# Kernel optimization log

Measured on AMD Instinct MI355X. Metric: run time of the kernel, lower is better.

Reference implementation:

```python
import jax, jax.numpy as jnp
import numpy as np

TOKEN_SELF_ATTN_VALUE = -50000.0
EPS_NORM = 1e-12
EPS_SCATTER = 1e-5
COMMITMENT = 1e-4


def _l2norm(x):
    return x / jnp.maximum(jnp.linalg.norm(x, axis=-1, keepdims=True), EPS_NORM)


def _shift(x):
    # relative-position shift, faithful to the torch `shift` helper
    # x: [..., i, j] -> [..., i, j]
    *pre, i, j = x.shape
    x = jnp.concatenate([x, jnp.zeros((*pre, i, i), x.dtype)], axis=-1)  # [..., i, i+j]
    l = i + j - 1
    x = x.reshape(*pre, i * (i + j))
    pad = (-x.shape[-1]) % l
    x = jnp.concatenate([x, jnp.zeros((*pre, pad), x.dtype)], axis=-1)
    x = x.reshape(*pre, -1, l)
    return x[..., :i, i - 1:]


def setup_inputs() -> dict:
    key = jax.random.key(0)
    k1, k2, k3, k4 = jax.random.split(key, 4)
    b, h, t, d = 4, 8, 8192, 64
    c, wsz = 64, 128
    qk = jax.random.normal(k1, (b, h, t, d), jnp.float32)
    v = jax.random.normal(k2, (b, h, t, d), jnp.float32)
    means = jax.random.normal(k3, (h, c, d), jnp.float32)
    means = _l2norm(means)  # trained kmeans means are unit-normalized
    rel_w = jax.random.normal(k4, (wsz, h, d), jnp.float32) * 0.02
    return {"qk": qk, "v": v, "means": means, "rel_w": rel_w}


def reference(qk, v, means, rel_w):
    b, h, t, d = qk.shape
    c = means.shape[1]
    wsz = min(rel_w.shape[0], t)

    # ---- kmeans routing (eval path: no iterations, fixed means) ----
    k_routing = _l2norm(qk)                                   # [b,h,t,d]
    dists = jnp.einsum('bhld,hcd->bhlc', k_routing, means)    # cosine sims
    buckets = jnp.argmax(dists, axis=-1)                      # [b,h,t]
    # top-wsz tokens per cluster, sorted ascending (matches topk -> sort -> transpose)
    _, idx = jax.lax.top_k(jnp.swapaxes(dists, -1, -2), wsz)  # [b,h,c,wsz]
    indices = jnp.sort(idx, axis=-1).reshape(b, h, c * wsz)   # [b,h,c*wsz]

    # commitment loss against routed means (means is a non-trainable buffer)
    routed_means = means[jnp.arange(h)[None, :, None], buckets]  # [b,h,t,d]
    loss = jnp.mean((k_routing - routed_means) ** 2) * COMMITMENT

    # ---- gather routed windows ----
    qk_g = jnp.take_along_axis(qk, indices[..., None], axis=2).reshape(b, h, c, wsz, d)
    v_g = jnp.take_along_axis(v, indices[..., None], axis=2).reshape(b, h, c, wsz, d)
    q = qk_g
    k = _l2norm(qk_g)

    scale = d ** -0.5
    dots = jnp.einsum('bhnid,bhnjd->bhnij', q, k) * scale     # [b,h,c,wsz,wsz]
    rel = jnp.einsum('bhnid,jhd->bhnij', q, rel_w) * scale
    dots = dots + _shift(rel)

    # token cannot attend to itself within its window
    eye = jnp.eye(wsz, dtype=bool)
    dots = jnp.where(eye, TOKEN_SELF_ATTN_VALUE, dots)

    attn = jax.nn.softmax(dots, axis=-1)
    bo = jnp.einsum('bhnij,bhnjd->bhnid', attn, v_g).reshape(b, h, c * wsz, d)

    # ---- scatter-mean back to original token positions ----
    def scat(idx1, src1):  # idx1: [N], src1: [N,d]
        num = jnp.zeros((t, d), src1.dtype).at[idx1].add(src1)
        den = jnp.zeros((t, d), src1.dtype).at[idx1].add(jnp.ones_like(src1))
        return num / (den + EPS_SCATTER)

    out = jax.vmap(jax.vmap(scat))(indices, bo)               # [b,h,t,d]
    return out, loss
```

## Files before the change

kernel.cpp:

```cpp
#include <hip/hip_runtime.h>
#include <hip/hip_bf16.h>
#include <math.h>

#define NB 4
#define NH 8
#define TT 8192
#define DD 64
#define NC 64
#define WW 128
#define BHN 32
#define SCALE 0.125f
#define INVCAP 24
#define DTPB 64

typedef __bf16  bf16x8 __attribute__((ext_vector_type(8)));
typedef __bf16  bf16x4 __attribute__((ext_vector_type(4)));
typedef float   f32x4  __attribute__((ext_vector_type(4)));
typedef unsigned long long u64;
typedef unsigned int u32;

#define MFMA(a, b, c) __builtin_amdgcn_mfma_f32_16x16x32_bf16((a), (b), (c), 0, 0, 0)

__device__ __forceinline__ u32 monokey(float f) {
    const u32 u = __float_as_uint(f);
    return u ^ (((u32)((int)u >> 31)) | 0x80000000u);
}

#define QD_ADDR(row, gi) (((row) << 6) + ((((gi) ^ ((row) & 7))) << 3))

__global__ __launch_bounds__(256) void k_dists(
    const float* __restrict__ qk, const float* __restrict__ means,
    const float* __restrict__ rel_w, __bf16* __restrict__ relb,
    u32* __restrict__ keys, double* __restrict__ lossa)
{
    __shared__ __attribute__((aligned(16))) __bf16 qh[64 * 64], qm[64 * 64], ql[64 * 64];
    __shared__ __attribute__((aligned(16))) __bf16 ah[64 * 64], am[64 * 64], al[64 * 64];
    __shared__ float invS[DTPB], s2S[DTPB], mn2S[NC];
    __shared__ double red[4];

    const int bh = blockIdx.x, h = bh & 7, tid = threadIdx.x;
    const int t0 = blockIdx.y * DTPB;

    if (blockIdx.y == 0) {
        const float4* rw = (const float4*)rel_w;
#pragma unroll
        for (int k = 0; k < 2; k++) {
            const int i = bh * 512 + k * 256 + tid;
            const float4 v = rw[i];
            bf16x4 o;
            o[0] = (__bf16)v.x; o[1] = (__bf16)v.y; o[2] = (__bf16)v.z; o[3] = (__bf16)v.w;
            *(bf16x4*)(relb + i * 4) = o;
        }
    }

    {
        const int r = tid >> 2, qt = tid & 3;
        const float4* src = (const float4*)(means + (size_t)(h * NC + r) * DD + qt * 16);
        float4 f[4];
        f[0] = src[0]; f[1] = src[1]; f[2] = src[2]; f[3] = src[3];
        bf16x8 vh[2], vm[2], vl[2];
        float ssq = 0.f;
#pragma unroll
        for (int j = 0; j < 16; j++) {
            const float xx = ((const float*)f)[j];
            ssq = fmaf(xx, xx, ssq);
            const __bf16 hh_ = (__bf16)xx;
            const float r1 = xx - (float)hh_;
            const __bf16 mm_ = (__bf16)r1;
            const float r2 = r1 - (float)mm_;
            vh[j >> 3][j & 7] = hh_; vm[j >> 3][j & 7] = mm_; vl[j >> 3][j & 7] = (__bf16)r2;
        }
#pragma unroll
        for (int gg = 0; gg < 2; gg++) {
            const int dst = QD_ADDR(r, qt * 2 + gg);
            *(bf16x8*)(ah + dst) = vh[gg];
            *(bf16x8*)(am + dst) = vm[gg];
            *(bf16x8*)(al + dst) = vl[gg];
        }
        ssq += __shfl_xor(ssq, 1);
        ssq += __shfl_xor(ssq, 2);
        if (qt == 0) mn2S[r] = ssq;
    }
    {
        const int r = tid >> 2, qt = tid & 3;
        const float4* src = (const float4*)(qk + ((size_t)bh * TT + t0 + r) * DD + qt * 16);
        float4 f[4];
        f[0] = src[0]; f[1] = src[1]; f[2] = src[2]; f[3] = src[3];
        bf16x8 vh[2], vm[2], vl[2];
        float ssq = 0.f;
#pragma unroll
        for (int j = 0; j < 16; j++) {
            const float xx = ((const float*)f)[j];
            ssq = fmaf(xx, xx, ssq);
            const __bf16 hh_ = (__bf16)xx;
            const float r1 = xx - (float)hh_;
            const __bf16 mm_ = (__bf16)r1;
            const float r2 = r1 - (float)mm_;
            vh[j >> 3][j & 7] = hh_; vm[j >> 3][j & 7] = mm_; vl[j >> 3][j & 7] = (__bf16)r2;
        }
#pragma unroll
        for (int gg = 0; gg < 2; gg++) {
            const int dst = QD_ADDR(r, qt * 2 + gg);
            *(bf16x8*)(qh + dst) = vh[gg];
            *(bf16x8*)(qm + dst) = vm[gg];
            *(bf16x8*)(ql + dst) = vl[gg];
        }
        ssq += __shfl_xor(ssq, 1);
        ssq += __shfl_xor(ssq, 2);
        if (qt == 0) {
            const float inv = 1.0f / fmaxf(sqrtf(ssq), 1e-12f);
            invS[r] = inv;
            s2S[r] = ssq * inv * inv;
        }
    }
    __syncthreads();

    const int lane = tid & 63, wv = tid >> 6;
    const int lo = lane & 15, quad = lane >> 4;

    bf16x8 Bh[2], Bm[2], Bl[2];
    {
        const int row = wv * 16 + lo;
#pragma unroll
        for (int kh = 0; kh < 2; kh++) {
            const int src = QD_ADDR(row, kh * 4 + quad);
            Bh[kh] = *(const bf16x8*)(qh + src);
            Bm[kh] = *(const bf16x8*)(qm + src);
            Bl[kh] = *(const bf16x8*)(ql + src);
        }
    }

    f32x4 acc[4];
#pragma unroll
    for (int ct = 0; ct < 4; ct++) {
        bf16x8 Ah[2], Am[2], Al[2];
#pragma unroll
        for (int kh = 0; kh < 2; kh++) {
            const int src = QD_ADDR(ct * 16 + lo, kh * 4 + quad);
            Ah[kh] = *(const bf16x8*)(ah + src);
            Am[kh] = *(const bf16x8*)(am + src);
            Al[kh] = *(const bf16x8*)(al + src);
        }
        f32x4 a = (f32x4){0.f, 0.f, 0.f, 0.f};
        a = MFMA(Al[0], Bm[0], a); a = MFMA(Al[1], Bm[1], a);
        a = MFMA(Am[0], Bl[0], a); a = MFMA(Am[1], Bl[1], a);
        a = MFMA(Am[0], Bm[0], a); a = MFMA(Am[1], Bm[1], a);
        a = MFMA(Ah[0], Bl[0], a); a = MFMA(Ah[1], Bl[1], a);
        a = MFMA(Al[0], Bh[0], a); a = MFMA(Al[1], Bh[1], a);
        a = MFMA(Am[0], Bh[0], a); a = MFMA(Am[1], Bh[1], a);
        a = MFMA(Ah[0], Bm[0], a); a = MFMA(Ah[1], Bm[1], a);
        a = MFMA(Ah[0], Bh[0], a); a = MFMA(Ah[1], Bh[1], a);
        acc[ct] = a;
    }

    const int tok = wv * 16 + lo;
    const float inv = invS[tok];
    float rawmax = -3.0e38f; int cbest = 0;
    u32* kout = keys + (size_t)bh * NC * TT + (size_t)(t0 + tok);
#pragma unroll
    for (int ct = 0; ct < 4; ct++)
#pragma unroll
        for (int r = 0; r < 4; r++) {
            const float raw = acc[ct][r];
            const int c = ct * 16 + quad * 4 + r;
            if (raw > rawmax) { rawmax = raw; cbest = c; }
            kout[(size_t)c * TT] = monokey(raw * inv);
        }

#pragma unroll
    for (int off = 16; off < 64; off <<= 1) {
        const float ov = __shfl_xor(rawmax, off);
        const int   oc = __shfl_xor(cbest, off);
        if (ov > rawmax || (ov == rawmax && oc < cbest)) { rawmax = ov; cbest = oc; }
    }
    double lt_lane = 0.0;
    if (quad == 0)
        lt_lane = (double)(s2S[tok] + mn2S[cbest] - 2.0f * rawmax * inv);

#pragma unroll
    for (int o = 32; o; o >>= 1) lt_lane += __shfl_xor(lt_lane, o);
    if (lane == 0) red[wv] = lt_lane;
    __syncthreads();
    if (tid == 0) atomicAdd(lossa, red[0] + red[1] + red[2] + red[3]);
}

__global__ __launch_bounds__(256) void k_topk(
    const u32* __restrict__ keys, int* __restrict__ indices,
    unsigned int* __restrict__ cnt, unsigned short* __restrict__ inv)
{
    __shared__ unsigned int hist[4][256];
    __shared__ int wsum[8];
    __shared__ int bc_bin, bc_rank, bc_cnt;

    const int bhc = blockIdx.x, tid = threadIdx.x;
    const int wv = tid >> 6, lane = tid & 63;
    const int bh = bhc >> 6;

    u32 key[32];
    {
        const uint4* p = (const uint4*)(keys + (size_t)bhc * TT + tid * 32);
#pragma unroll
        for (int i = 0; i < 8; i++) {
            uint4 u = p[i];
            key[4*i] = u.x; key[4*i+1] = u.y; key[4*i+2] = u.z; key[4*i+3] = u.w;
        }
    }

    u32 thr = 0;
    int need = 128, gshift = 24, prevShift = 0;
    unsigned int* hb = &hist[0][0];

    for (int level = 0; level < 4; level++) {
        const int shift = 24 - 8 * level;
        hb[tid] = 0; hb[tid + 256] = 0; hb[tid + 512] = 0; hb[tid + 768] = 0;
        __syncthreads();
        unsigned int* hw = hist[wv];
        if (level == 0) {
#pragma unroll
            for (int i = 0; i < 32; i++)
                atomicAdd(&hw[key[i] >> 24], 1u);
        } else {
            const u32 pv = thr >> prevShift;
#pragma unroll
            for (int i = 0; i < 32; i++)
                if ((key[i] >> prevShift) == pv)
                    atomicAdd(&hw[(key[i] >> shift) & 255u], 1u);
        }
        __syncthreads();

        const int b = 255 - tid;
        const int c = hist[0][b] + hist[1][b] + hist[2][b] + hist[3][b];
        int incl = c;
#pragma unroll
        for (int o = 1; o < 64; o <<= 1) {
            const int v = __shfl_up(incl, o);
            if (lane >= o) incl += v;
        }
        if (lane == 63) wsum[wv] = incl;
        __syncthreads();
        int above = incl - c;
        for (int wj = 0; wj < wv; wj++) above += wsum[wj];
        if (above < need && above + c >= need) {
            bc_bin = b; bc_rank = above; bc_cnt = c;
        }
        __syncthreads();
        thr |= ((u32)bc_bin) << shift;
        need -= bc_rank;
        gshift = shift;
        prevShift = shift;
        if (bc_cnt == need || shift == 0) break;
    }

    const u32 tg = thr >> gshift;
    int cgt = 0, ceq = 0;
#pragma unroll
    for (int i = 0; i < 32; i++) {
        const u32 kg = key[i] >> gshift;
        cgt += (kg > tg) ? 1 : 0;
        ceq += (kg == tg) ? 1 : 0;
    }
    int ig = cgt, ie = ceq;
#pragma unroll
    for (int o = 1; o < 64; o <<= 1) {
        const int vg = __shfl_up(ig, o);
        const int ve = __shfl_up(ie, o);
        if (lane >= o) { ig += vg; ie += ve; }
    }
    if (lane == 63) { wsum[wv] = ig; wsum[4 + wv] = ie; }
    __syncthreads();
    int pgt = ig - cgt, peq = ie - ceq;
    for (int wj = 0; wj < wv; wj++) { pgt += wsum[wj]; peq += wsum[4 + wj]; }

    const int rneed = need;
    int* outp = indices + bhc * WW;
    unsigned int* cntb = cnt + (bh << 13);
    unsigned short* invb = inv + (((size_t)bh << 13) * INVCAP);
    const int cbase = (bhc & 63) * WW;
    int g = 0, e = 0;
#pragma unroll
    for (int i = 0; i < 32; i++) {
        const int tok = tid * 32 + i;
        const u32 kg = key[i] >> gshift;
        if (kg > tg) {
            const int tb = (peq + e < rneed) ? (peq + e) : rneed;
            const int wpos = pgt + g + tb;
            outp[wpos] = tok;
            const unsigned int pos = atomicAdd(&cntb[tok], 1u);
            if (pos < INVCAP) invb[(size_t)tok * INVCAP + pos] = (unsigned short)(cbase + wpos);
            g++;
        } else if (kg == tg) {
            if (peq + e < rneed) {
                const int wpos = pgt + g + peq + e;
                outp[wpos] = tok;
                const unsigned int pos = atomicAdd(&cntb[tok], 1u);
                if (pos < INVCAP) invb[(size_t)tok * INVCAP + pos] = (unsigned short)(cbase + wpos);
            }
            e++;
        }
    }
}

#define QS_ADDR(row, gi) (((row) << 6) + ((((gi) ^ ((row) & 7))) << 3))

__global__ __launch_bounds__(512) void k_attn(
    const float* __restrict__ qk, const float* __restrict__ vin,
    const __bf16* __restrict__ relb, const int* __restrict__ indices,
    float* __restrict__ bo)
{
    __shared__ __attribute__((aligned(16))) __bf16 uv[64 * 136];
    __shared__ __attribute__((aligned(16))) __bf16 rs[128 * 136];
    __shared__ float invs[128];

    const int tid  = threadIdx.x;
    const int lane = tid & 63;
    const int wv   = tid >> 6;
    const int lo   = lane & 15;
    const int quad = lane >> 4;
    const int rbase = wv * 16;

    const int bhc = blockIdx.x;
    const int bh  = bhc >> 6;
    const int h   = bh & 7;

    const int r  = tid >> 2;
    const int qp = tid & 3;
    const int rowidx = indices[bhc * WW + r];
    const size_t rowoff = ((size_t)bh * TT + rowidx) * DD + qp * 16;
    float4 q0, q1, q2, q3, vreg[4];
    {
        const float4* qsrc = (const float4*)(qk + rowoff);
        q0 = qsrc[0]; q1 = qsrc[1]; q2 = qsrc[2]; q3 = qsrc[3];
        const float4* vsrc = (const float4*)(vin + rowoff);
        vreg[0] = vsrc[0]; vreg[1] = vsrc[1]; vreg[2] = vsrc[2]; vreg[3] = vsrc[3];
    }
    {
        float ssq = q0.x*q0.x + q0.y*q0.y + q0.z*q0.z + q0.w*q0.w
                  + q1.x*q1.x + q1.y*q1.y + q1.z*q1.z + q1.w*q1.w
                  + q2.x*q2.x + q2.y*q2.y + q2.z*q2.z + q2.w*q2.w
                  + q3.x*q3.x + q3.y*q3.y + q3.z*q3.z + q3.w*q3.w;
        ssq += __shfl_xor(ssq, 1);
        ssq += __shfl_xor(ssq, 2);
        if (qp == 0) invs[r] = 1.0f / fmaxf(sqrtf(ssq), 1e-12f);
        bf16x8 va, vb;
        va[0]=(__bf16)q0.x; va[1]=(__bf16)q0.y; va[2]=(__bf16)q0.z; va[3]=(__bf16)q0.w;
        va[4]=(__bf16)q1.x; va[5]=(__bf16)q1.y; va[6]=(__bf16)q1.z; va[7]=(__bf16)q1.w;
        vb[0]=(__bf16)q2.x; vb[1]=(__bf16)q2.y; vb[2]=(__bf16)q2.z; vb[3]=(__bf16)q2.w;
        vb[4]=(__bf16)q3.x; vb[5]=(__bf16)q3.y; vb[6]=(__bf16)q3.z; vb[7]=(__bf16)q3.w;
        *(bf16x8*)(uv + QS_ADDR(r, qp * 2))     = va;
        *(bf16x8*)(uv + QS_ADDR(r, qp * 2 + 1)) = vb;
    }
    __syncthreads();

    f32x4 acc[8];

#pragma unroll
    for (int nt = 0; nt < 8; nt++) acc[nt] = (f32x4){0.f, 0.f, 0.f, 0.f};
#pragma unroll
    for (int k0 = 0; k0 < 64; k0 += 32) {
        bf16x8 qa = *(const bf16x8*)(uv + QS_ADDR(rbase + lo, (k0 >> 3) + quad));
#pragma unroll
        for (int nt = 0; nt < 8; nt++) {
            const bf16x8 wb = *(const bf16x8*)(relb + ((nt * 16 + lo) * 8 + h) * 64 + k0 + quad * 8);
            acc[nt] = MFMA(qa, wb, acc[nt]);
        }
    }
#pragma unroll
    for (int nt = 0; nt < 8; nt++)
#pragma unroll
        for (int rg = 0; rg < 4; rg++)
            rs[(rbase + quad * 4 + rg) * 136 + nt * 16 + lo] = (__bf16)acc[nt][rg];

#pragma unroll
    for (int nt = 0; nt < 8; nt++) acc[nt] = (f32x4){0.f, 0.f, 0.f, 0.f};
#pragma unroll
    for (int k0 = 0; k0 < 64; k0 += 32) {
        bf16x8 qa = *(const bf16x8*)(uv + QS_ADDR(rbase + lo, (k0 >> 3) + quad));
#pragma unroll
        for (int nt = 0; nt < 8; nt++) {
            bf16x8 qb = *(const bf16x8*)(uv + QS_ADDR(nt * 16 + lo, (k0 >> 3) + quad));
            acc[nt] = MFMA(qa, qb, acc[nt]);
        }
    }

    float inv_j[8];
#pragma unroll
    for (int nt = 0; nt < 8; nt++) inv_j[nt] = invs[nt * 16 + lo];

#pragma unroll
    for (int rg = 0; rg < 4; rg++) {
        const int i = rbase + quad * 4 + rg;
#pragma unroll
        for (int nt = 0; nt < 8; nt++) {
            const int j = nt * 16 + lo;
            float val = acc[nt][rg] * inv_j[nt] * SCALE;
            if (j <= i) val += SCALE * (float)rs[i * 136 + (j + 127 - i)];
            if (j == i) val = -50000.0f;
            acc[nt][rg] = val;
        }
    }

#pragma unroll
    for (int rg = 0; rg < 4; rg++) {
        float m = -3.0e38f;
#pragma unroll
        for (int nt = 0; nt < 8; nt++) m = fmaxf(m, acc[nt][rg]);
#pragma unroll
        for (int msk = 1; msk < 16; msk <<= 1) m = fmaxf(m, __shfl_xor(m, msk));
        float s = 0.f;
#pragma unroll
        for (int nt = 0; nt < 8; nt++) {
            const float e = __expf(acc[nt][rg] - m);
            acc[nt][rg] = e; s += e;
        }
#pragma unroll
        for (int msk = 1; msk < 16; msk <<= 1) s += __shfl_xor(s, msk);
        const float is = 1.0f / s;
        const int i = rbase + quad * 4 + rg;
#pragma unroll
        for (int nt = 0; nt < 8; nt++)
            rs[i * 136 + nt * 16 + lo] = (__bf16)(acc[nt][rg] * is);
    }
    __syncthreads();

    __bf16* vt = uv;
#pragma unroll
    for (int i = 0; i < 4; i++) {
        vt[(qp * 16 + 4*i + 0) * 136 + r] = (__bf16)vreg[i].x;
        vt[(qp * 16 + 4*i + 1) * 136 + r] = (__bf16)vreg[i].y;
        vt[(qp * 16 + 4*i + 2) * 136 + r] = (__bf16)vreg[i].z;
        vt[(qp * 16 + 4*i + 3) * 136 + r] = (__bf16)vreg[i].w;
    }
    __syncthreads();

    f32x4 accO[4];
#pragma unroll
    for (int nt = 0; nt < 4; nt++) accO[nt] = (f32x4){0.f, 0.f, 0.f, 0.f};
#pragma unroll
    for (int k0 = 0; k0 < 128; k0 += 32) {
        bf16x8 pa = *(const bf16x8*)(rs + (rbase + lo) * 136 + k0 + quad * 8);
#pragma unroll
        for (int nt = 0; nt < 4; nt++) {
            bf16x8 vb = *(const bf16x8*)(vt + (nt * 16 + lo) * 136 + k0 + quad * 8);
            accO[nt] = MFMA(pa, vb, accO[nt]);
        }
    }

    float* bb = bo + (size_t)bhc * (WW * DD);
#pragma unroll
    for (int rg = 0; rg < 4; rg++) {
        const int i = rbase + quad * 4 + rg;
#pragma unroll
        for (int nt = 0; nt < 4; nt++)
            bb[(size_t)i * DD + nt * 16 + lo] = accO[nt][rg];
    }
}

__global__ __launch_bounds__(256) void k_out(
    const float* __restrict__ bo, const unsigned int* __restrict__ cnt,
    const unsigned short* __restrict__ inv, const double* __restrict__ lossa,
    float* __restrict__ out)
{
    const int tid = threadIdx.x;
    const int g = blockIdx.x * 16 + (tid >> 4);
    const int l = tid & 15;
    const int bh = g >> 13;
    const unsigned int n = cnt[g];
    const int nc = (n < (unsigned)INVCAP) ? (int)n : INVCAP;
    const unsigned short* ip = inv + (size_t)g * INVCAP;
    const float* bbase = bo + (((size_t)bh << 13) * DD) + l * 4;

    const uint4 ipv = *(const uint4*)ip;
    const int s0 = ipv.x & 0xffff, s1 = ipv.x >> 16;
    const int s2 = ipv.y & 0xffff, s3 = ipv.y >> 16;
    const int s4 = ipv.z & 0xffff, s5 = ipv.z >> 16;
    const int s6 = ipv.w & 0xffff, s7 = ipv.w >> 16;

    float4 a0 = {0.f,0.f,0.f,0.f}, a1 = a0, a2 = a0, a3 = a0;
    float4 a4 = a0, a5 = a0, a6 = a0, a7 = a0;
    if (nc > 0) a0 = *(const float4*)(bbase + (size_t)s0 * DD);
    if (nc > 1) a1 = *(const float4*)(bbase + (size_t)s1 * DD);
    if (nc > 2) a2 = *(const float4*)(bbase + (size_t)s2 * DD);
    if (nc > 3) a3 = *(const float4*)(bbase + (size_t)s3 * DD);
    if (nc > 4) a4 = *(const float4*)(bbase + (size_t)s4 * DD);
    if (nc > 5) a5 = *(const float4*)(bbase + (size_t)s5 * DD);
    if (nc > 6) a6 = *(const float4*)(bbase + (size_t)s6 * DD);
    if (nc > 7) a7 = *(const float4*)(bbase + (size_t)s7 * DD);

    float4 s;
    s.x = ((a0.x + a1.x) + (a2.x + a3.x)) + ((a4.x + a5.x) + (a6.x + a7.x));
    s.y = ((a0.y + a1.y) + (a2.y + a3.y)) + ((a4.y + a5.y) + (a6.y + a7.y));
    s.z = ((a0.z + a1.z) + (a2.z + a3.z)) + ((a4.z + a5.z) + (a6.z + a7.z));
    s.w = ((a0.w + a1.w) + (a2.w + a3.w)) + ((a4.w + a5.w) + (a6.w + a7.w));

    for (int e = 8; e < nc; e++) {
        const int slot = ip[e];
        const float4 v4 = *(const float4*)(bbase + (size_t)slot * DD);
        s.x += v4.x; s.y += v4.y; s.z += v4.z; s.w += v4.w;
    }

    const float r = 1.0f / ((float)n + 1e-5f);
    s.x *= r; s.y *= r; s.z *= r; s.w *= r;
    *(float4*)(out + (size_t)g * DD + l * 4) = s;
    if (g == 0 && l == 0) out[16777216] = (float)(lossa[0] * (0.0001 / 16777216.0));
}

extern "C" void kernel_launch(void* const* d_in, const int* in_sizes, int n_in,
                              void* d_out, int out_size, void* d_ws, size_t ws_size,
                              hipStream_t stream) {
    (void)in_sizes; (void)n_in; (void)ws_size; (void)out_size;
    const float* qk    = (const float*)d_in[0];
    const float* v     = (const float*)d_in[1];
    const float* means = (const float*)d_in[2];
    const float* rel_w = (const float*)d_in[3];
    float* out = (float*)d_out;

    char* ws = (char*)d_ws;
    const size_t KEYS_B = (size_t)BHN * NC * TT * 4;
    const size_t IDX_B  = (size_t)BHN * NC * WW * 4;
    const size_t CNT_B  = (size_t)BHN * TT * 4;
    const size_t INV_B  = (size_t)BHN * TT * INVCAP * 2;
    u32*            keys  = (u32*)ws;
    float*          bo    = (float*)ws;
    int*            idx   = (int*)(ws + KEYS_B);
    unsigned int*   cnt   = (unsigned int*)(ws + KEYS_B + IDX_B);
    double*         lossa = (double*)(ws + KEYS_B + IDX_B + CNT_B);
    unsigned short* inv   = (unsigned short*)(ws + KEYS_B + IDX_B + CNT_B + 4096);
    __bf16*         relb  = (__bf16*)(ws + KEYS_B + IDX_B + CNT_B + 4096 + INV_B);

    hipMemsetAsync(ws + KEYS_B + IDX_B, 0, CNT_B + 4096, stream);

    k_dists<<<dim3(BHN, TT / DTPB), 256, 0, stream>>>(qk, means, rel_w, relb, keys, lossa);
    k_topk<<<BHN * NC, 256, 0, stream>>>(keys, idx, cnt, inv);
    k_attn<<<BHN * NC, 512, 0, stream>>>(qk, v, relb, idx, bo);
    k_out<<<BHN * TT / 16, 256, 0, stream>>>(bo, cnt, inv, lossa, out);
}
```

Baseline: 336.7 us.

## Shrink attention kernel LDS with packed triangular rel buffer and split P

The relative-position scores are now stored in a packed lower-triangular layout, so only the entries the shift actually uses are kept, and that buffer is reused later for transposed V. The probability matrix stays in registers and is written to LDS in two 64-column halves, with two PV MFMA passes. Together these cut the block's shared-memory footprint so more blocks can be resident per CU. A min-occupancy hint in the launch bounds adds register pressure and a risk of spills, plus some extra address arithmetic and LDS writes.

```diff
diff --git a/kernel.cpp b/kernel.cpp
--- a/kernel.cpp
+++ b/kernel.cpp
@@ -302,13 +302,13 @@
 
 #define QS_ADDR(row, gi) (((row) << 6) + ((((gi) ^ ((row) & 7))) << 3))
 
-__global__ __launch_bounds__(512) void k_attn(
+__global__ __launch_bounds__(512, 8) void k_attn(
     const float* __restrict__ qk, const float* __restrict__ vin,
     const __bf16* __restrict__ relb, const int* __restrict__ indices,
     float* __restrict__ bo)
 {
-    __shared__ __attribute__((aligned(16))) __bf16 uv[64 * 136];
-    __shared__ __attribute__((aligned(16))) __bf16 rs[128 * 136];
+    __shared__ __attribute__((aligned(16))) __bf16 u1[128 * 72];
+    __shared__ __attribute__((aligned(16))) __bf16 u2[64 * 136];
     __shared__ float invs[128];
 
     const int tid  = threadIdx.x;
@@ -326,14 +326,14 @@
     const int qp = tid & 3;
     const int rowidx = indices[bhc * WW + r];
     const size_t rowoff = ((size_t)bh * TT + rowidx) * DD + qp * 16;
-    float4 q0, q1, q2, q3, vreg[4];
+    float4 vreg[4];
     {
+        float4 q0, q1, q2, q3;
         const float4* qsrc = (const float4*)(qk + rowoff);
         q0 = qsrc[0]; q1 = qsrc[1]; q2 = qsrc[2]; q3 = qsrc[3];
         const float4* vsrc = (const float4*)(vin + rowoff);
         vreg[0] = vsrc[0]; vreg[1] = vsrc[1]; vreg[2] = vsrc[2]; vreg[3] = vsrc[3];
-    }
-    {
+
         float ssq = q0.x*q0.x + q0.y*q0.y + q0.z*q0.z + q0.w*q0.w
                   + q1.x*q1.x + q1.y*q1.y + q1.z*q1.z + q1.w*q1.w
                   + q2.x*q2.x + q2.y*q2.y + q2.z*q2.z + q2.w*q2.w
@@ -346,8 +346,8 @@
         va[4]=(__bf16)q1.x; va[5]=(__bf16)q1.y; va[6]=(__bf16)q1.z; va[7]=(__bf16)q1.w;
         vb[0]=(__bf16)q2.x; vb[1]=(__bf16)q2.y; vb[2]=(__bf16)q2.z; vb[3]=(__bf16)q2.w;
         vb[4]=(__bf16)q3.x; vb[5]=(__bf16)q3.y; vb[6]=(__bf16)q3.z; vb[7]=(__bf16)q3.w;
-        *(bf16x8*)(uv + QS_ADDR(r, qp * 2))     = va;
-        *(bf16x8*)(uv + QS_ADDR(r, qp * 2 + 1)) = vb;
+        *(bf16x8*)(u1 + QS_ADDR(r, qp * 2))     = va;
+        *(bf16x8*)(u1 + QS_ADDR(r, qp * 2 + 1)) = vb;
     }
     __syncthreads();
 
@@ -357,7 +357,7 @@
     for (int nt = 0; nt < 8; nt++) acc[nt] = (f32x4){0.f, 0.f, 0.f, 0.f};
 #pragma unroll
     for (int k0 = 0; k0 < 64; k0 += 32) {
-        bf16x8 qa = *(const bf16x8*)(uv + QS_ADDR(rbase + lo, (k0 >> 3) + quad));
+        bf16x8 qa = *(const bf16x8*)(u1 + QS_ADDR(rbase + lo, (k0 >> 3) + quad));
 #pragma unroll
         for (int nt = 0; nt < 8; nt++) {
             const bf16x8 wb = *(const bf16x8*)(relb + ((nt * 16 + lo) * 8 + h) * 64 + k0 + quad * 8);
@@ -367,33 +367,34 @@
 #pragma unroll
     for (int nt = 0; nt < 8; nt++)
 #pragma unroll
-        for (int rg = 0; rg < 4; rg++)
-            rs[(rbase + quad * 4 + rg) * 136 + nt * 16 + lo] = (__bf16)acc[nt][rg];
+        for (int rg = 0; rg < 4; rg++) {
+            const int i = rbase + quad * 4 + rg;
+            const int jsrc = nt * 16 + lo - 127 + i;
+            if (jsrc >= 0)
+                u2[((i * (i + 1)) >> 1) + jsrc] = (__bf16)acc[nt][rg];
+        }
 
 #pragma unroll
     for (int nt = 0; nt < 8; nt++) acc[nt] = (f32x4){0.f, 0.f, 0.f, 0.f};
 #pragma unroll
     for (int k0 = 0; k0 < 64; k0 += 32) {
-        bf16x8 qa = *(const bf16x8*)(uv + QS_ADDR(rbase + lo, (k0 >> 3) + quad));
+        bf16x8 qa = *(const bf16x8*)(u1 + QS_ADDR(rbase + lo, (k0 >> 3) + quad));
 #pragma unroll
         for (int nt = 0; nt < 8; nt++) {
-            bf16x8 qb = *(const bf16x8*)(uv + QS_ADDR(nt * 16 + lo, (k0 >> 3) + quad));
+            bf16x8 qb = *(const bf16x8*)(u1 + QS_ADDR(nt * 16 + lo, (k0 >> 3) + quad));
             acc[nt] = MFMA(qa, qb, acc[nt]);
         }
     }
-
-    float inv_j[8];
-#pragma unroll
-    for (int nt = 0; nt < 8; nt++) inv_j[nt] = invs[nt * 16 + lo];
 
 #pragma unroll
     for (int rg = 0; rg < 4; rg++) {
         const int i = rbase + quad * 4 + rg;
+        const int off = (i * (i + 1)) >> 1;
 #pragma unroll
         for (int nt = 0; nt < 8; nt++) {
             const int j = nt * 16 + lo;
-            float val = acc[nt][rg] * inv_j[nt] * SCALE;
-            if (j <= i) val += SCALE * (float)rs[i * 136 + (j + 127 - i)];
+            float val = acc[nt][rg] * invs[j] * SCALE;
+            if (j <= i) val += SCALE * (float)u2[off + j];
             if (j == i) val = -50000.0f;
             acc[nt][rg] = val;
         }
@@ -415,14 +416,12 @@
 #pragma unroll
         for (int msk = 1; msk < 16; msk <<= 1) s += __shfl_xor(s, msk);
         const float is = 1.0f / s;
-        const int i = rbase + quad * 4 + rg;
-#pragma unroll
-        for (int nt = 0; nt < 8; nt++)
-            rs[i * 136 + nt * 16 + lo] = (__bf16)(acc[nt][rg] * is);
+#pragma unroll
+        for (int nt = 0; nt < 8; nt++) acc[nt][rg] *= is;
     }
     __syncthreads();
 
-    __bf16* vt = uv;
+    __bf16* vt = u2;
 #pragma unroll
     for (int i = 0; i < 4; i++) {
         vt[(qp * 16 + 4*i + 0) * 136 + r] = (__bf16)vreg[i].x;
@@ -430,17 +429,38 @@
         vt[(qp * 16 + 4*i + 2) * 136 + r] = (__bf16)vreg[i].z;
         vt[(qp * 16 + 4*i + 3) * 136 + r] = (__bf16)vreg[i].w;
     }
+#pragma unroll
+    for (int nt = 0; nt < 4; nt++)
+#pragma unroll
+        for (int rg = 0; rg < 4; rg++)
+            u1[(rbase + quad * 4 + rg) * 72 + nt * 16 + lo] = (__bf16)acc[nt][rg];
     __syncthreads();
 
     f32x4 accO[4];
 #pragma unroll
     for (int nt = 0; nt < 4; nt++) accO[nt] = (f32x4){0.f, 0.f, 0.f, 0.f};
 #pragma unroll
-    for (int k0 = 0; k0 < 128; k0 += 32) {
-        bf16x8 pa = *(const bf16x8*)(rs + (rbase + lo) * 136 + k0 + quad * 8);
+    for (int k0 = 0; k0 < 64; k0 += 32) {
+        bf16x8 pa = *(const bf16x8*)(u1 + (rbase + lo) * 72 + k0 + quad * 8);
 #pragma unroll
         for (int nt = 0; nt < 4; nt++) {
             bf16x8 vb = *(const bf16x8*)(vt + (nt * 16 + lo) * 136 + k0 + quad * 8);
+            accO[nt] = MFMA(pa, vb, accO[nt]);
+        }
+    }
+
+#pragma unroll
+    for (int nt = 4; nt < 8; nt++)
+#pragma unroll
+        for (int rg = 0; rg < 4; rg++)
+            u1[(rbase + quad * 4 + rg) * 72 + (nt - 4) * 16 + lo] = (__bf16)acc[nt][rg];
+
+#pragma unroll
+    for (int k0 = 0; k0 < 64; k0 += 32) {
+        bf16x8 pa = *(const bf16x8*)(u1 + (rbase + lo) * 72 + k0 + quad * 8);
+#pragma unroll
+        for (int nt = 0; nt < 4; nt++) {
+            bf16x8 vb = *(const bf16x8*)(vt + (nt * 16 + lo) * 136 + 64 + k0 + quad * 8);
             accO[nt] = MFMA(pa, vb, accO[nt]);
         }
     }
```

After: 363.7 us. 8.0% more time.
